# Kernel optimization log

Measured on AMD Instinct MI355X. Metric: run time of the kernel, lower is better.

## Reference

```python
import jax, jax.numpy as jnp
import numpy as np

B, A, EH, DH, H, W = 32, 512, 256, 384, 64, 64  # batch, attn_size, enc_hs, dec_hs, spatial


def setup_inputs() -> dict:
    key = jax.random.key(0)
    ks = jax.random.split(key, 5)
    return {
        "dec_h": jax.random.normal(ks[0], (B, DH), jnp.float32),
        "weighted_enc_out": jax.random.normal(ks[1], (B, A, H, W), jnp.float32),
        "enc_out": jax.random.normal(ks[2], (B, EH, H, W), jnp.float32),
        # decoder_linear: Linear(dec_hs -> attn_size)
        "W_dec": jax.random.normal(ks[3], (A, DH), jnp.float32) / np.sqrt(DH).astype(np.float32),
        "b_dec": jnp.zeros((A,), jnp.float32),
        # energy_layer: Conv2d(attn_size -> 1, kernel 1x1) == per-pixel dot with a vector
        "w_energy": jax.random.normal(ks[4], (A,), jnp.float32) / np.sqrt(A).astype(np.float32),
        "b_energy": jnp.zeros((), jnp.float32),
    }


def reference(dec_h, weighted_enc_out, enc_out, W_dec, b_dec, w_energy, b_energy):
    # decoder_linear(dec_h): [B, DH] -> [B, A]
    dec_proj = dec_h @ W_dec.T + b_dec
    # broadcast add over spatial dims + tanh: [B, A, H, W]
    pre_scores = jnp.tanh(weighted_enc_out + dec_proj[:, :, None, None])
    # 1x1 conv to 1 channel == contraction over channel axis: [B, H, W]
    scores = jnp.einsum('bahw,a->bhw', pre_scores, w_energy) + b_energy
    # softmax over flattened spatial dims
    b, h, w = scores.shape
    alphas = jax.nn.softmax(scores.reshape(b, h * w), axis=1).reshape(b, h, w)
    # weighted sum of encoder features: [B, EH]
    context = jnp.einsum('bchw,bhw->bc', enc_out, alphas)
    return context, alphas
```

## Files before the change

kernel.cpp:

```cpp
#include <hip/hip_runtime.h>
#include <math.h>

#define B  32
#define A  512
#define EH 256
#define DH 384
#define HW 4096
#define NCHUNK 8
#define ACH (A / NCHUNK)
#define P4 (HW / 4)

__global__ void k_decproj(const float* __restrict__ dec_h,
                          const float* __restrict__ W_dec,
                          const float* __restrict__ b_dec,
                          float* __restrict__ dec_proj) {
    int wave = (blockIdx.x * blockDim.x + threadIdx.x) >> 6;
    int lane = threadIdx.x & 63;
    if (wave >= B * A) return;
    int b = wave >> 9;
    int a = wave & 511;
    const float* dh = dec_h + b * DH;
    const float* wd = W_dec + a * DH;
    float acc = 0.f;
    for (int k = lane; k < DH; k += 64)
        acc += dh[k] * wd[k];
    #pragma unroll
    for (int s = 32; s > 0; s >>= 1)
        acc += __shfl_down(acc, s);
    if (lane == 0) dec_proj[wave] = acc + b_dec[a];
}

__global__ void k_scores_part(const float* __restrict__ weo,
                              const float* __restrict__ dec_proj,
                              const float* __restrict__ w_energy,
                              float* __restrict__ partial) {
    __shared__ float s_dp[ACH];
    __shared__ float s_we[ACH];
    const int b  = blockIdx.z;
    const int a0 = blockIdx.y * ACH;
    const int p4 = blockIdx.x * blockDim.x + threadIdx.x;
    const float C = 2.8853900817779268f;

    if (threadIdx.x < ACH) {
        s_dp[threadIdx.x] = dec_proj[b * A + a0 + threadIdx.x] * C;
        s_we[threadIdx.x] = w_energy[a0 + threadIdx.x];
    }
    __syncthreads();

    const float4* w4 = (const float4*)(weo + ((size_t)b * A + a0) * HW);
    float4 acc = make_float4(0.f, 0.f, 0.f, 0.f);
    #pragma unroll 8
    for (int a = 0; a < ACH; ++a) {
        float4 x = w4[(size_t)a * P4 + p4];
        float dp = s_dp[a];
        float we = s_we[a];
        float rx = __builtin_amdgcn_rcpf(__builtin_amdgcn_exp2f(fmaf(x.x, C, dp)) + 1.f);
        float ry = __builtin_amdgcn_rcpf(__builtin_amdgcn_exp2f(fmaf(x.y, C, dp)) + 1.f);
        float rz = __builtin_amdgcn_rcpf(__builtin_amdgcn_exp2f(fmaf(x.z, C, dp)) + 1.f);
        float rw = __builtin_amdgcn_rcpf(__builtin_amdgcn_exp2f(fmaf(x.w, C, dp)) + 1.f);
        acc.x = fmaf(we, fmaf(-2.f, rx, 1.f), acc.x);
        acc.y = fmaf(we, fmaf(-2.f, ry, 1.f), acc.y);
        acc.z = fmaf(we, fmaf(-2.f, rz, 1.f), acc.z);
        acc.w = fmaf(we, fmaf(-2.f, rw, 1.f), acc.w);
    }
    float4* out4 = (float4*)partial;
    out4[((size_t)(b * NCHUNK + blockIdx.y)) * P4 + p4] = acc;
}

__global__ void k_softmax(const float* __restrict__ partial,
                          const float* __restrict__ b_energy,
                          float* __restrict__ alphas) {
    __shared__ float red[256];
    const int b = blockIdx.x;
    const float be = b_energy[0];
    float vals[16];
    float m = -INFINITY;
    #pragma unroll
    for (int i = 0; i < 16; ++i) {
        int p = threadIdx.x + i * 256;
        float s = be;
        #pragma unroll
        for (int c = 0; c < NCHUNK; ++c)
            s += partial[((size_t)(b * NCHUNK + c) << 12) + p];
        vals[i] = s;
        m = fmaxf(m, s);
    }
    red[threadIdx.x] = m; __syncthreads();
    for (int s2 = 128; s2 > 0; s2 >>= 1) {
        if (threadIdx.x < s2)
            red[threadIdx.x] = fmaxf(red[threadIdx.x], red[threadIdx.x + s2]);
        __syncthreads();
    }
    m = red[0]; __syncthreads();
    float sum = 0.f;
    #pragma unroll
    for (int i = 0; i < 16; ++i) { vals[i] = __expf(vals[i] - m); sum += vals[i]; }
    red[threadIdx.x] = sum; __syncthreads();
    for (int s2 = 128; s2 > 0; s2 >>= 1) {
        if (threadIdx.x < s2)
            red[threadIdx.x] += red[threadIdx.x + s2];
        __syncthreads();
    }
    const float inv = 1.f / red[0];
    float* out = alphas + b * HW;
    #pragma unroll
    for (int i = 0; i < 16; ++i)
        out[threadIdx.x + i * 256] = vals[i] * inv;
}

__global__ void k_context(const float* __restrict__ enc,
                          const float* __restrict__ alphas,
                          float* __restrict__ context) {
    const int b = blockIdx.y;
    const int wave = threadIdx.x >> 6;
    const int lane = threadIdx.x & 63;
    const int c = blockIdx.x * 4 + wave;
    const float4* e4 = (const float4*)(enc + ((size_t)b * EH + c) * HW);
    const float4* a4 = (const float4*)(alphas + (size_t)b * HW);
    float acc = 0.f;
    #pragma unroll
    for (int it = 0; it < 16; ++it) {
        float4 v  = e4[it * 64 + lane];
        float4 al = a4[it * 64 + lane];
        acc += v.x * al.x + v.y * al.y + v.z * al.z + v.w * al.w;
    }
    #pragma unroll
    for (int s = 32; s > 0; s >>= 1)
        acc += __shfl_down(acc, s);
    if (lane == 0) context[b * EH + c] = acc;
}

extern "C" void kernel_launch(void* const* d_in, const int* in_sizes, int n_in,
                              void* d_out, int out_size, void* d_ws, size_t ws_size,
                              hipStream_t stream) {
    const float* dec_h = (const float*)d_in[0];
    const float* weo   = (const float*)d_in[1];
    const float* enc   = (const float*)d_in[2];
    const float* W_dec = (const float*)d_in[3];
    const float* b_dec = (const float*)d_in[4];
    const float* w_en  = (const float*)d_in[5];
    const float* b_en  = (const float*)d_in[6];

    float* context = (float*)d_out;
    float* alphas  = context + B * EH;

    float* dec_proj = (float*)d_ws;
    float* partial  = dec_proj + B * A;

    k_decproj<<<dim3((B * A) / 4), 256, 0, stream>>>(dec_h, W_dec, b_dec, dec_proj);
    k_scores_part<<<dim3(P4 / 256, NCHUNK, B), 256, 0, stream>>>(weo, dec_proj, w_en, partial);
    k_softmax<<<dim3(B), 256, 0, stream>>>(partial, b_en, alphas);
    k_context<<<dim3(EH / 4, B), 256, 0, stream>>>(enc, alphas, context);
}
```

Before: 450.0 us.

## Split score chunks finer and widen softmax to 1024 threads with float4

Result: no change. 450.6 us (+0.1%).

```diff
diff --git a/kernel.cpp b/kernel.cpp
--- a/kernel.cpp
+++ b/kernel.cpp
@@ -6,7 +6,7 @@
 #define EH 256
 #define DH 384
 #define HW 4096
-#define NCHUNK 8
+#define NCHUNK 16
 #define ACH (A / NCHUNK)
 #define P4 (HW / 4)
 
@@ -30,10 +30,11 @@
     if (lane == 0) dec_proj[wave] = acc + b_dec[a];
 }
 
-__global__ void k_scores_part(const float* __restrict__ weo,
-                              const float* __restrict__ dec_proj,
-                              const float* __restrict__ w_energy,
-                              float* __restrict__ partial) {
+__global__ __launch_bounds__(256, 8)
+void k_scores_part(const float* __restrict__ weo,
+                   const float* __restrict__ dec_proj,
+                   const float* __restrict__ w_energy,
+                   float* __restrict__ partial) {
     __shared__ float s_dp[ACH];
     __shared__ float s_we[ACH];
     const int b  = blockIdx.z;
@@ -70,42 +71,36 @@
 __global__ void k_softmax(const float* __restrict__ partial,
                           const float* __restrict__ b_energy,
                           float* __restrict__ alphas) {
-    __shared__ float red[256];
+    __shared__ float red[1024];
     const int b = blockIdx.x;
+    const int t = threadIdx.x;
     const float be = b_energy[0];
-    float vals[16];
-    float m = -INFINITY;
+    const float4* pp = (const float4*)partial;
+
+    float4 s = make_float4(be, be, be, be);
     #pragma unroll
-    for (int i = 0; i < 16; ++i) {
-        int p = threadIdx.x + i * 256;
-        float s = be;
-        #pragma unroll
-        for (int c = 0; c < NCHUNK; ++c)
-            s += partial[((size_t)(b * NCHUNK + c) << 12) + p];
-        vals[i] = s;
-        m = fmaxf(m, s);
+    for (int c = 0; c < NCHUNK; ++c) {
+        float4 v = pp[((size_t)(b * NCHUNK + c)) * P4 + t];
+        s.x += v.x; s.y += v.y; s.z += v.z; s.w += v.w;
     }
-    red[threadIdx.x] = m; __syncthreads();
-    for (int s2 = 128; s2 > 0; s2 >>= 1) {
-        if (threadIdx.x < s2)
-            red[threadIdx.x] = fmaxf(red[threadIdx.x], red[threadIdx.x + s2]);
+    float m = fmaxf(fmaxf(s.x, s.y), fmaxf(s.z, s.w));
+    red[t] = m; __syncthreads();
+    for (int s2 = 512; s2 > 0; s2 >>= 1) {
+        if (t < s2) red[t] = fmaxf(red[t], red[t + s2]);
         __syncthreads();
     }
     m = red[0]; __syncthreads();
-    float sum = 0.f;
-    #pragma unroll
-    for (int i = 0; i < 16; ++i) { vals[i] = __expf(vals[i] - m); sum += vals[i]; }
-    red[threadIdx.x] = sum; __syncthreads();
-    for (int s2 = 128; s2 > 0; s2 >>= 1) {
-        if (threadIdx.x < s2)
-            red[threadIdx.x] += red[threadIdx.x + s2];
+    float4 e;
+    e.x = __expf(s.x - m); e.y = __expf(s.y - m);
+    e.z = __expf(s.z - m); e.w = __expf(s.w - m);
+    red[t] = e.x + e.y + e.z + e.w; __syncthreads();
+    for (int s2 = 512; s2 > 0; s2 >>= 1) {
+        if (t < s2) red[t] += red[t + s2];
         __syncthreads();
     }
     const float inv = 1.f / red[0];
-    float* out = alphas + b * HW;
-    #pragma unroll
-    for (int i = 0; i < 16; ++i)
-        out[threadIdx.x + i * 256] = vals[i] * inv;
+    e.x *= inv; e.y *= inv; e.z *= inv; e.w *= inv;
+    ((float4*)(alphas + b * HW))[t] = e;
 }
 
 __global__ void k_context(const float* __restrict__ enc,
@@ -149,6 +144,6 @@
 
     k_decproj<<<dim3((B * A) / 4), 256, 0, stream>>>(dec_h, W_dec, b_dec, dec_proj);
     k_scores_part<<<dim3(P4 / 256, NCHUNK, B), 256, 0, stream>>>(weo, dec_proj, w_en, partial);
-    k_softmax<<<dim3(B), 256, 0, stream>>>(partial, b_en, alphas);
+    k_softmax<<<dim3(B), 1024, 0, stream>>>(partial, b_en, alphas);
     k_context<<<dim3(EH / 4, B), 256, 0, stream>>>(enc, alphas, context);
 }
```
